# Performance work log

Measured on AMD Instinct MI355X. Metric: run time of the kernel, lower is better.

## Reference

```python
import jax, jax.numpy as jnp
import numpy as np

H = 256       # hidden_dim
E = H // 2    # operator embedding dim
T = 12        # num_tempers
O = 3         # num_ops per temper
HOPS = 4      # max_path_hops
B = 128       # batch
D = 2048      # input_dim
NCLS = 10     # task_head classes


def setup_inputs() -> dict:
    key = jax.random.key(0)
    ks = jax.random.split(key, 12)
    x = jax.random.normal(ks[0], (B, D), jnp.float32)
    N = B * (D // H)  # 1024 patch tokens
    # per-hop routed temper per patch; value == T means halt
    sampled_tempers = jax.random.randint(ks[1], (HOPS, N), 0, T + 1, jnp.int32)
    sampled_ops = jax.random.randint(ks[2], (HOPS, N), 0, O, jnp.int32)
    s1 = 1.0 / np.sqrt(H + E)
    W1 = jax.random.uniform(ks[3], (T, O, H + E, H), jnp.float32, -s1, s1)
    b1 = jax.random.uniform(ks[4], (T, O, H), jnp.float32, -s1, s1)
    s2 = 1.0 / np.sqrt(H)
    W2 = jax.random.uniform(ks[5], (T, O, H, H), jnp.float32, -s2, s2)
    b2 = jax.random.uniform(ks[6], (T, O, H), jnp.float32, -s2, s2)
    op_emb = jax.random.normal(ks[7], (T, O, E), jnp.float32)
    ln_g = jnp.ones((H,), jnp.float32)
    ln_b = jnp.zeros((H,), jnp.float32)
    Wt = jax.random.uniform(ks[8], (H, NCLS), jnp.float32, -s2, s2)
    bt = jax.random.uniform(ks[9], (NCLS,), jnp.float32, -s2, s2)
    return dict(x=x, W1=W1, b1=b1, W2=W2, b2=b2, op_emb=op_emb,
                ln_g=ln_g, ln_b=ln_b, Wt=Wt, bt=bt,
                sampled_tempers=sampled_tempers, sampled_ops=sampled_ops)


def reference(x, W1, b1, W2, b2, op_emb, ln_g, ln_b, Wt, bt,
              sampled_tempers, sampled_ops):
    Bsz, Din = x.shape
    pad = (-Din) % H
    if pad > 0:
        x = jnp.pad(x, ((0, 0), (0, pad)))
    state = x.reshape(-1, H)                       # [N, H] patch states
    active = jnp.ones((state.shape[0],), bool)     # not-yet-halted mask
    for hop in range(HOPS):
        t = sampled_tempers[hop]
        o = sampled_ops[hop]
        active = active & (t != T)                 # T == halt action
        tc = jnp.clip(t, 0, T - 1)                 # safe index for halted rows
        emb = op_emb[tc, o]                        # [N, E] op embedding gather
        xa = jnp.concatenate([state, emb], axis=-1)  # [N, H+E]
        # per-token expert weight gather + batched matvec (memory-bound dispatch)
        h = jax.nn.relu(jnp.einsum('ni,nio->no', xa, W1[tc, o]) + b1[tc, o])
        y = jax.nn.relu(jnp.einsum('ni,nio->no', h, W2[tc, o]) + b2[tc, o])
        state = jnp.where(active[:, None], y, state)
    pooled = state.reshape(Bsz, -1, H).mean(axis=1)   # [B, H]
    mu = pooled.mean(axis=-1, keepdims=True)
    var = pooled.var(axis=-1, keepdims=True)
    normed = (pooled - mu) * jax.lax.rsqrt(var + 1e-5) * ln_g + ln_b
    return normed @ Wt + bt                           # [B, 10]
```

## Files before the change

kernel.cpp:

```cpp
#include <hip/hip_runtime.h>

typedef __attribute__((ext_vector_type(8))) short short8;
typedef __attribute__((ext_vector_type(4))) float floatx4;

#define NEXP   36
#define NTOK   1024
#define HOPS   4

#define OFF_STATE   0u
#define OFF_W1B     1048576u
#define OFF_W2B     5767168u
#define OFF_C1      10485760u
#define OFF_COUNTS  10522624u
#define OFF_LISTS   10523264u
#define OFF_JOBS    11113088u
#define OFF_NJ      11115136u

__device__ __forceinline__ unsigned short f2bf(float f) {
    unsigned u = __float_as_uint(f);
    u += 0x7FFFu + ((u >> 16) & 1u);
    return (unsigned short)(u >> 16);
}

__global__ __launch_bounds__(256) void prep_kernel(
    const float* __restrict__ W1, const float* __restrict__ b1,
    const float* __restrict__ W2, const float* __restrict__ op_emb,
    const int* __restrict__ tempers, const int* __restrict__ ops,
    unsigned short* __restrict__ W1b, unsigned short* __restrict__ W2b,
    float* __restrict__ c1, int* __restrict__ counts, int* __restrict__ lists,
    int* __restrict__ jobs, int* __restrict__ njobs)
{
    const int bid = blockIdx.x;
    const int t = threadIdx.x;

    if (bid < 2304) {
        const int mat = bid / 1152;
        const int id  = bid % 1152;
        const int e   = id / 32;
        const int sub = id % 32;
        const int kb  = sub / 4;
        const int jt  = sub % 4;
        const float* src = mat ? (W2 + e * 65536) : (W1 + e * 98304);
        unsigned short* dst = (mat ? W2b : W1b) + e * 65536;
        const int j  = jt * 64 + (t & 63);
        const int ks = (t >> 6) * 8;
        short8 v;
        #pragma unroll
        for (int i = 0; i < 8; i++)
            v[i] = (short)f2bf(src[(kb * 32 + ks + i) * 256 + j]);
        *(short8*)(dst + (kb * 256 + j) * 32 + ks) = v;
    } else if (bid < 2340) {
        const int e = bid - 2304;
        __shared__ float eb[128];
        if (t < 128) eb[t] = op_emb[e * 128 + t];
        __syncthreads();
        float acc = b1[e * 256 + t];
        const float* wp = W1 + e * 98304 + 256 * 256;
        #pragma unroll 4
        for (int k = 0; k < 128; k++)
            acc += eb[k] * wp[k * 256 + t];
        c1[e * 256 + t] = acc;
    } else {
        __shared__ int lc[HOPS * NEXP];
        if (t < HOPS * NEXP) lc[t] = 0;
        __syncthreads();
        for (int q = 0; q < 4; q++) {
            int n = q * 256 + t;
            bool act = true;
            for (int hop = 0; hop < HOPS; hop++) {
                int tt = tempers[hop * NTOK + n];
                int oo = ops[hop * NTOK + n];
                act = act && (tt != 12);
                if (act) {
                    int e = tt * 3 + oo;
                    int pos = atomicAdd(&lc[hop * NEXP + e], 1);
                    lists[(hop * NEXP + e) * NTOK + pos] = n;
                }
            }
        }
        __syncthreads();
        if (t < HOPS * NEXP) counts[t] = lc[t];
        if (t < HOPS) {
            int hop = t, nj = 0;
            for (int e = 0; e < NEXP; e++) {
                int c = lc[hop * NEXP + e];
                for (int m0 = 0; m0 < c; m0 += 16)
                    jobs[hop * 128 + nj++] = (m0 << 8) | e;
            }
            njobs[hop] = nj;
        }
    }
}

__global__ __launch_bounds__(1024, 4) void hop_kernel(
    const float* __restrict__ src, float* __restrict__ state,
    const unsigned short* __restrict__ W1b,
    const unsigned short* __restrict__ W2b,
    const float* __restrict__ c1, const float* __restrict__ b2,
    const int* __restrict__ counts, const int* __restrict__ lists,
    const int* __restrict__ jobs, const int* __restrict__ njobs, int hop)
{
    if (blockIdx.x >= njobs[hop]) return;
    const int job = jobs[hop * 128 + blockIdx.x];
    const int e   = job & 0xFF;
    const int m0  = job >> 8;
    const int n_e = counts[hop * NEXP + e];
    const int mact = min(16, n_e - m0);

    const int t = threadIdx.x;
    const int l = t & 63, w = t >> 6;
    const int col = l & 15, g = l >> 4;
    const int j = w * 16 + col;

    const unsigned short* Wp  = W1b + e * 65536;
    const unsigned short* Wp2 = W2b + e * 65536;
    short8 B1[8], B2[8];
    #pragma unroll
    for (int kb = 0; kb < 8; kb++) {
        B1[kb] = *(const short8*)(Wp  + (kb * 256 + j) * 32 + g * 8);
        B2[kb] = *(const short8*)(Wp2 + (kb * 256 + j) * 32 + g * 8);
    }
    const float cv = c1[e * 256 + j];
    const float bv = b2[e * 256 + j];

    __shared__ int toks[16];
    __shared__ unsigned short Ab[4096];
    __shared__ unsigned short Hb[4096];

    if (t < 16) toks[t] = (t < mact) ? lists[(hop * NEXP + e) * NTOK + m0 + t] : 0;
    __syncthreads();

    {
        int m = t >> 6;
        int k = (t & 63) * 4;
        float4 v = make_float4(0.f, 0.f, 0.f, 0.f);
        if (m < mact) v = *(const float4*)(src + toks[m] * 256 + k);
        int kb = k >> 5, gg = (k >> 3) & 3, i = k & 7;
        unsigned short* d = Ab + kb * 512 + (gg * 16 + m) * 8 + i;
        d[0] = f2bf(v.x); d[1] = f2bf(v.y); d[2] = f2bf(v.z); d[3] = f2bf(v.w);
    }
    __syncthreads();

    floatx4 acc = (floatx4){cv, cv, cv, cv};
    #pragma unroll
    for (int kb = 0; kb < 8; kb++) {
        short8 a = *(const short8*)(Ab + kb * 512 + l * 8);
        acc = __builtin_amdgcn_mfma_f32_16x16x32_bf16(a, B1[kb], acc, 0, 0, 0);
    }
    {
        int kb2 = j >> 5, g2 = (j >> 3) & 3, i2 = j & 7;
        #pragma unroll
        for (int r = 0; r < 4; r++) {
            int m = g * 4 + r;
            float vv = acc[r];
            vv = vv > 0.f ? vv : 0.f;
            Hb[kb2 * 512 + (g2 * 16 + m) * 8 + i2] = f2bf(vv);
        }
    }
    __syncthreads();

    floatx4 acc2 = (floatx4){bv, bv, bv, bv};
    #pragma unroll
    for (int kb = 0; kb < 8; kb++) {
        short8 a = *(const short8*)(Hb + kb * 512 + l * 8);
        acc2 = __builtin_amdgcn_mfma_f32_16x16x32_bf16(a, B2[kb], acc2, 0, 0, 0);
    }
    #pragma unroll
    for (int r = 0; r < 4; r++) {
        int m = g * 4 + r;
        if (m < mact) {
            float vv = acc2[r];
            state[toks[m] * 256 + j] = vv > 0.f ? vv : 0.f;
        }
    }
}

__global__ __launch_bounds__(256) void final_kernel(
    const float* __restrict__ x, const float* __restrict__ state,
    const int* __restrict__ tempers,
    const float* __restrict__ ln_g, const float* __restrict__ ln_b,
    const float* __restrict__ Wt, const float* __restrict__ bt,
    float* __restrict__ out)
{
    const int b = blockIdx.x, t = threadIdx.x;
    float s = 0.f;
    #pragma unroll
    for (int p = 0; p < 8; p++) {
        int n = b * 8 + p;
        const float* rowsrc = (tempers[n] != 12) ? state : x;
        s += rowsrc[n * 256 + t];
    }
    s *= 0.125f;

    float v1 = s, v2 = s * s;
    #pragma unroll
    for (int off = 32; off; off >>= 1) {
        v1 += __shfl_down(v1, off);
        v2 += __shfl_down(v2, off);
    }
    __shared__ float red[8];
    __shared__ float stats[2];
    const int w = t >> 6, l = t & 63;
    if (l == 0) { red[w] = v1; red[4 + w] = v2; }
    __syncthreads();
    if (t == 0) {
        float su = red[0] + red[1] + red[2] + red[3];
        float sq = red[4] + red[5] + red[6] + red[7];
        float mu = su * (1.0f / 256.0f);
        float var = sq * (1.0f / 256.0f) - mu * mu;
        stats[0] = mu;
        stats[1] = rsqrtf(var + 1e-5f);
    }
    __syncthreads();
    float normed = (s - stats[0]) * stats[1] * ln_g[t] + ln_b[t];

    __shared__ float pr[40];
    #pragma unroll
    for (int c = 0; c < 10; c++) {
        float pv = normed * Wt[t * 10 + c];
        #pragma unroll
        for (int off = 32; off; off >>= 1) pv += __shfl_down(pv, off);
        if (l == 0) pr[w * 10 + c] = pv;
    }
    __syncthreads();
    if (t < 10)
        out[b * 10 + t] = pr[t] + pr[10 + t] + pr[20 + t] + pr[30 + t] + bt[t];
}

extern "C" void kernel_launch(void* const* d_in, const int* in_sizes, int n_in,
                              void* d_out, int out_size, void* d_ws, size_t ws_size,
                              hipStream_t stream)
{
    const float* x      = (const float*)d_in[0];
    const float* W1     = (const float*)d_in[1];
    const float* b1     = (const float*)d_in[2];
    const float* W2     = (const float*)d_in[3];
    const float* b2     = (const float*)d_in[4];
    const float* op_emb = (const float*)d_in[5];
    const float* ln_g   = (const float*)d_in[6];
    const float* ln_b   = (const float*)d_in[7];
    const float* Wt     = (const float*)d_in[8];
    const float* bt     = (const float*)d_in[9];
    const int* tempers  = (const int*)d_in[10];
    const int* ops      = (const int*)d_in[11];

    char* ws = (char*)d_ws;
    float* state          = (float*)(ws + OFF_STATE);
    unsigned short* W1b   = (unsigned short*)(ws + OFF_W1B);
    unsigned short* W2b   = (unsigned short*)(ws + OFF_W2B);
    float* c1             = (float*)(ws + OFF_C1);
    int* counts           = (int*)(ws + OFF_COUNTS);
    int* lists            = (int*)(ws + OFF_LISTS);
    int* jobs             = (int*)(ws + OFF_JOBS);
    int* njobs            = (int*)(ws + OFF_NJ);
    float* out            = (float*)d_out;

    prep_kernel<<<2341, 256, 0, stream>>>(W1, b1, W2, op_emb, tempers, ops,
                                          W1b, W2b, c1, counts, lists,
                                          jobs, njobs);
    for (int hop = 0; hop < HOPS; hop++)
        hop_kernel<<<128, 1024, 0, stream>>>(hop == 0 ? x : state, state,
                                             W1b, W2b, c1, b2,
                                             counts, lists, jobs, njobs, hop);
    final_kernel<<<128, 256, 0, stream>>>(x, state, tempers,
                                          ln_g, ln_b, Wt, bt, out);
}
```

Measured before the change: 140.9 us.

## Fuse hop and final kernels into one persistent kernel with per-token progress flags

The four per-hop launches and the final pooling/LN/head kernel are replaced by a single 256-block kernel in which 64 blocks are assigned to each hop. Instead of kernel boundaries, each job spins on per-token progress counters with acquire loads and publishes completion with release stores, so later hops can start on tokens as soon as their previous-hop update is done. The final head waits on each token's last-active-hop count. This removes launch gaps and global barriers, but it relies on all 256 blocks being co-resident to avoid deadlock, and the spin-waits plus fences add overhead.

```diff
diff --git a/kernel.cpp b/kernel.cpp
--- a/kernel.cpp
+++ b/kernel.cpp
@@ -15,6 +15,8 @@
 #define OFF_LISTS   10523264u
 #define OFF_JOBS    11113088u
 #define OFF_NJ      11115136u
+#define OFF_PROG    11115152u
+#define OFF_FINV    11119248u
 
 __device__ __forceinline__ unsigned short f2bf(float f) {
     unsigned u = __float_as_uint(f);
@@ -28,7 +30,8 @@
     const int* __restrict__ tempers, const int* __restrict__ ops,
     unsigned short* __restrict__ W1b, unsigned short* __restrict__ W2b,
     float* __restrict__ c1, int* __restrict__ counts, int* __restrict__ lists,
-    int* __restrict__ jobs, int* __restrict__ njobs)
+    int* __restrict__ jobs, int* __restrict__ njobs,
+    int* __restrict__ prog, int* __restrict__ finv)
 {
     const int bid = blockIdx.x;
     const int t = threadIdx.x;
@@ -66,7 +69,9 @@
         __syncthreads();
         for (int q = 0; q < 4; q++) {
             int n = q * 256 + t;
+            prog[n] = 0;
             bool act = true;
+            int la = 0;
             for (int hop = 0; hop < HOPS; hop++) {
                 int tt = tempers[hop * NTOK + n];
                 int oo = ops[hop * NTOK + n];
@@ -75,8 +80,10 @@
                     int e = tt * 3 + oo;
                     int pos = atomicAdd(&lc[hop * NEXP + e], 1);
                     lists[(hop * NEXP + e) * NTOK + pos] = n;
+                    la = hop + 1;
                 }
             }
+            finv[n] = la;
         }
         __syncthreads();
         if (t < HOPS * NEXP) counts[t] = lc[t];
@@ -92,116 +99,150 @@
     }
 }
 
-__global__ __launch_bounds__(1024, 4) void hop_kernel(
-    const float* __restrict__ src, float* __restrict__ state,
+__global__ __launch_bounds__(1024, 4) void mega_kernel(
+    const float* __restrict__ x, float* __restrict__ state,
     const unsigned short* __restrict__ W1b,
     const unsigned short* __restrict__ W2b,
     const float* __restrict__ c1, const float* __restrict__ b2,
     const int* __restrict__ counts, const int* __restrict__ lists,
-    const int* __restrict__ jobs, const int* __restrict__ njobs, int hop)
+    const int* __restrict__ jobs, const int* __restrict__ njobs,
+    int* __restrict__ prog, const int* __restrict__ finv,
+    const float* __restrict__ ln_g, const float* __restrict__ ln_b,
+    const float* __restrict__ Wt, const float* __restrict__ bt,
+    float* __restrict__ out)
 {
-    if (blockIdx.x >= njobs[hop]) return;
-    const int job = jobs[hop * 128 + blockIdx.x];
-    const int e   = job & 0xFF;
-    const int m0  = job >> 8;
-    const int n_e = counts[hop * NEXP + e];
-    const int mact = min(16, n_e - m0);
+    const int hop  = blockIdx.x >> 6;
+    const int slot = blockIdx.x & 63;
+    const int nj   = njobs[hop];
 
     const int t = threadIdx.x;
     const int l = t & 63, w = t >> 6;
     const int col = l & 15, g = l >> 4;
     const int j = w * 16 + col;
 
-    const unsigned short* Wp  = W1b + e * 65536;
-    const unsigned short* Wp2 = W2b + e * 65536;
-    short8 B1[8], B2[8];
-    #pragma unroll
-    for (int kb = 0; kb < 8; kb++) {
-        B1[kb] = *(const short8*)(Wp  + (kb * 256 + j) * 32 + g * 8);
-        B2[kb] = *(const short8*)(Wp2 + (kb * 256 + j) * 32 + g * 8);
-    }
-    const float cv = c1[e * 256 + j];
-    const float bv = b2[e * 256 + j];
-
     __shared__ int toks[16];
     __shared__ unsigned short Ab[4096];
     __shared__ unsigned short Hb[4096];
 
-    if (t < 16) toks[t] = (t < mact) ? lists[(hop * NEXP + e) * NTOK + m0 + t] : 0;
-    __syncthreads();
-
-    {
-        int m = t >> 6;
-        int k = (t & 63) * 4;
-        float4 v = make_float4(0.f, 0.f, 0.f, 0.f);
-        if (m < mact) v = *(const float4*)(src + toks[m] * 256 + k);
-        int kb = k >> 5, gg = (k >> 3) & 3, i = k & 7;
-        unsigned short* d = Ab + kb * 512 + (gg * 16 + m) * 8 + i;
-        d[0] = f2bf(v.x); d[1] = f2bf(v.y); d[2] = f2bf(v.z); d[3] = f2bf(v.w);
-    }
-    __syncthreads();
-
-    floatx4 acc = (floatx4){cv, cv, cv, cv};
-    #pragma unroll
-    for (int kb = 0; kb < 8; kb++) {
-        short8 a = *(const short8*)(Ab + kb * 512 + l * 8);
-        acc = __builtin_amdgcn_mfma_f32_16x16x32_bf16(a, B1[kb], acc, 0, 0, 0);
-    }
-    {
-        int kb2 = j >> 5, g2 = (j >> 3) & 3, i2 = j & 7;
+    const float* asrc = (hop == 0) ? x : state;
+
+    for (int jb = slot; jb < nj; jb += 64) {
+        const int job = jobs[hop * 128 + jb];
+        const int e   = job & 0xFF;
+        const int m0  = job >> 8;
+        const int n_e = counts[hop * NEXP + e];
+        const int mact = min(16, n_e - m0);
+
+        const unsigned short* Wp  = W1b + e * 65536;
+        const unsigned short* Wp2 = W2b + e * 65536;
+        short8 B1[8], B2[8];
+        #pragma unroll
+        for (int kb = 0; kb < 8; kb++) {
+            B1[kb] = *(const short8*)(Wp  + (kb * 256 + j) * 32 + g * 8);
+            B2[kb] = *(const short8*)(Wp2 + (kb * 256 + j) * 32 + g * 8);
+        }
+        const float cv = c1[e * 256 + j];
+        const float bv = b2[e * 256 + j];
+
+        __syncthreads();
+        if (t < 16) {
+            int n = (t < mact) ? lists[(hop * NEXP + e) * NTOK + m0 + t] : 0;
+            toks[t] = n;
+            if (t < mact && hop > 0) {
+                while (__hip_atomic_load(&prog[n], __ATOMIC_ACQUIRE,
+                                         __HIP_MEMORY_SCOPE_AGENT) < hop)
+                    __builtin_amdgcn_s_sleep(1);
+            }
+        }
+        __syncthreads();
+
+        {
+            int m = t >> 6;
+            int k = (t & 63) * 4;
+            float4 v = make_float4(0.f, 0.f, 0.f, 0.f);
+            if (m < mact) v = *(const float4*)(asrc + toks[m] * 256 + k);
+            int kb = k >> 5, gg = (k >> 3) & 3, i = k & 7;
+            unsigned short* d = Ab + kb * 512 + (gg * 16 + m) * 8 + i;
+            d[0] = f2bf(v.x); d[1] = f2bf(v.y); d[2] = f2bf(v.z); d[3] = f2bf(v.w);
+        }
+        __syncthreads();
+
+        floatx4 acc = (floatx4){cv, cv, cv, cv};
+        #pragma unroll
+        for (int kb = 0; kb < 8; kb++) {
+            short8 a = *(const short8*)(Ab + kb * 512 + l * 8);
+            acc = __builtin_amdgcn_mfma_f32_16x16x32_bf16(a, B1[kb], acc, 0, 0, 0);
+        }
+        {
+            int kb2 = j >> 5, g2 = (j >> 3) & 3, i2 = j & 7;
+            #pragma unroll
+            for (int r = 0; r < 4; r++) {
+                int m = g * 4 + r;
+                float vv = acc[r];
+                vv = vv > 0.f ? vv : 0.f;
+                Hb[kb2 * 512 + (g2 * 16 + m) * 8 + i2] = f2bf(vv);
+            }
+        }
+        __syncthreads();
+
+        floatx4 acc2 = (floatx4){bv, bv, bv, bv};
+        #pragma unroll
+        for (int kb = 0; kb < 8; kb++) {
+            short8 a = *(const short8*)(Hb + kb * 512 + l * 8);
+            acc2 = __builtin_amdgcn_mfma_f32_16x16x32_bf16(a, B2[kb], acc2, 0, 0, 0);
+        }
         #pragma unroll
         for (int r = 0; r < 4; r++) {
             int m = g * 4 + r;
-            float vv = acc[r];
-            vv = vv > 0.f ? vv : 0.f;
-            Hb[kb2 * 512 + (g2 * 16 + m) * 8 + i2] = f2bf(vv);
+            if (m < mact) {
+                float vv = acc2[r];
+                state[toks[m] * 256 + j] = vv > 0.f ? vv : 0.f;
+            }
+        }
+
+        __syncthreads();
+        if (t < mact) {
+            __threadfence();
+            __hip_atomic_store(&prog[toks[t]], hop + 1,
+                               __ATOMIC_RELEASE, __HIP_MEMORY_SCOPE_AGENT);
+        }
+    }
+
+    const int b = blockIdx.x;
+    if (b >= 128) return;
+
+    if (t < 8) {
+        int n = b * 8 + t;
+        int need = finv[n];
+        if (need > 0) {
+            while (__hip_atomic_load(&prog[n], __ATOMIC_ACQUIRE,
+                                     __HIP_MEMORY_SCOPE_AGENT) < need)
+                __builtin_amdgcn_s_sleep(1);
         }
     }
     __syncthreads();
 
-    floatx4 acc2 = (floatx4){bv, bv, bv, bv};
-    #pragma unroll
-    for (int kb = 0; kb < 8; kb++) {
-        short8 a = *(const short8*)(Hb + kb * 512 + l * 8);
-        acc2 = __builtin_amdgcn_mfma_f32_16x16x32_bf16(a, B2[kb], acc2, 0, 0, 0);
-    }
-    #pragma unroll
-    for (int r = 0; r < 4; r++) {
-        int m = g * 4 + r;
-        if (m < mact) {
-            float vv = acc2[r];
-            state[toks[m] * 256 + j] = vv > 0.f ? vv : 0.f;
-        }
-    }
-}
-
-__global__ __launch_bounds__(256) void final_kernel(
-    const float* __restrict__ x, const float* __restrict__ state,
-    const int* __restrict__ tempers,
-    const float* __restrict__ ln_g, const float* __restrict__ ln_b,
-    const float* __restrict__ Wt, const float* __restrict__ bt,
-    float* __restrict__ out)
-{
-    const int b = blockIdx.x, t = threadIdx.x;
-    float s = 0.f;
-    #pragma unroll
-    for (int p = 0; p < 8; p++) {
-        int n = b * 8 + p;
-        const float* rowsrc = (tempers[n] != 12) ? state : x;
-        s += rowsrc[n * 256 + t];
-    }
-    s *= 0.125f;
-
-    float v1 = s, v2 = s * s;
-    #pragma unroll
-    for (int off = 32; off; off >>= 1) {
-        v1 += __shfl_down(v1, off);
-        v2 += __shfl_down(v2, off);
-    }
     __shared__ float red[8];
     __shared__ float stats[2];
-    const int w = t >> 6, l = t & 63;
-    if (l == 0) { red[w] = v1; red[4 + w] = v2; }
+    __shared__ float pr[40];
+
+    float s = 0.f;
+    if (t < 256) {
+        #pragma unroll
+        for (int p = 0; p < 8; p++) {
+            int n = b * 8 + p;
+            const float* rowsrc = (finv[n] > 0) ? state : x;
+            s += rowsrc[n * 256 + t];
+        }
+        s *= 0.125f;
+        float v1 = s, v2 = s * s;
+        #pragma unroll
+        for (int off = 32; off; off >>= 1) {
+            v1 += __shfl_down(v1, off);
+            v2 += __shfl_down(v2, off);
+        }
+        if ((t & 63) == 0) { red[t >> 6] = v1; red[4 + (t >> 6)] = v2; }
+    }
     __syncthreads();
     if (t == 0) {
         float su = red[0] + red[1] + red[2] + red[3];
@@ -212,15 +253,15 @@
         stats[1] = rsqrtf(var + 1e-5f);
     }
     __syncthreads();
-    float normed = (s - stats[0]) * stats[1] * ln_g[t] + ln_b[t];
-
-    __shared__ float pr[40];
-    #pragma unroll
-    for (int c = 0; c < 10; c++) {
-        float pv = normed * Wt[t * 10 + c];
-        #pragma unroll
-        for (int off = 32; off; off >>= 1) pv += __shfl_down(pv, off);
-        if (l == 0) pr[w * 10 + c] = pv;
+    if (t < 256) {
+        float normed = (s - stats[0]) * stats[1] * ln_g[t] + ln_b[t];
+        #pragma unroll
+        for (int c = 0; c < 10; c++) {
+            float pv = normed * Wt[t * 10 + c];
+            #pragma unroll
+            for (int off = 32; off; off >>= 1) pv += __shfl_down(pv, off);
+            if ((t & 63) == 0) pr[(t >> 6) * 10 + c] = pv;
+        }
     }
     __syncthreads();
     if (t < 10)
@@ -253,15 +294,15 @@
     int* lists            = (int*)(ws + OFF_LISTS);
     int* jobs             = (int*)(ws + OFF_JOBS);
     int* njobs            = (int*)(ws + OFF_NJ);
+    int* prog             = (int*)(ws + OFF_PROG);
+    int* finv             = (int*)(ws + OFF_FINV);
     float* out            = (float*)d_out;
 
     prep_kernel<<<2341, 256, 0, stream>>>(W1, b1, W2, op_emb, tempers, ops,
                                           W1b, W2b, c1, counts, lists,
-                                          jobs, njobs);
-    for (int hop = 0; hop < HOPS; hop++)
-        hop_kernel<<<128, 1024, 0, stream>>>(hop == 0 ? x : state, state,
-                                             W1b, W2b, c1, b2,
-                                             counts, lists, jobs, njobs, hop);
-    final_kernel<<<128, 256, 0, stream>>>(x, state, tempers,
+                                          jobs, njobs, prog, finv);
+    mega_kernel<<<256, 1024, 0, stream>>>(x, state, W1b, W2b, c1, b2,
+                                          counts, lists, jobs, njobs,
+                                          prog, finv,
                                           ln_g, ln_b, Wt, bt, out);
 }
```

Result: slower. 233.6 us (+65.8%).
